# Performance work log

Hardware: AMD Instinct MI355X
Metric: run time of the kernel (lower is better)

Reference implementation:

```python
import jax, jax.numpy as jnp
import numpy as np

B, N, U = 8, 2048, 256
BN_EPS = 1e-3  # keras BatchNormalization default epsilon
ADJ_DENSITY = 0.008  # ~16 neighbors per node on average


def setup_inputs() -> dict:
    key = jax.random.key(0)
    ks = jax.random.split(key, 16)
    s = 0.05  # weight scale ('random_normal' init is small-stddev in keras)
    x = jax.random.normal(ks[0], (B, N, U), jnp.float32)
    # sparse binary adjacency stored dense (per-sample SpMM pattern)
    adj = (jax.random.uniform(ks[1], (B, N, N)) < ADJ_DENSITY).astype(jnp.float32)
    nodal_mask = jnp.ones((B, N), jnp.float32)
    return {
        'x': x, 'adj': adj, 'nodal_mask': nodal_mask,
        'W_lin': jax.random.normal(ks[2], (U, U)) * s, 'b_lin': jnp.zeros((U,)),
        'Wq_mp': jax.random.normal(ks[3], (3, U, U)) * s, 'bq_mp': jnp.zeros((3, U)),
        'Wk_mp': jax.random.normal(ks[4], (3, U, U)) * s, 'bk_mp': jnp.zeros((3, U)),
        'Wv_mp': jax.random.normal(ks[5], (3, U, U)) * s, 'bv_mp': jnp.zeros((3, U)),
        'Wk_att': jax.random.normal(ks[6], (U, U)) * s,
        'Wv_att': jax.random.normal(ks[7], (U, U)) * s,
        'Wq_att': jax.random.normal(ks[8], (U, U)) * s,
        'Wo_att': jax.random.normal(ks[9], (U, U)) * s,
        'bn_gamma': jnp.ones((U,)), 'bn_beta': jnp.zeros((U,)),
        'bn_mean': jnp.zeros((U,)), 'bn_var': jnp.ones((U,)),
        'W_proj': jax.random.normal(ks[10], (U, U)) * s, 'b_proj': jnp.zeros((U,)),
        'W_res': jax.random.normal(ks[11], (U, U)) * s, 'b_res': jnp.zeros((U,)),
    }


def _dympn(x, adj, Ws, bs, mask):
    # 3 message-passing layers, each applied K_l=2 times (inference value)
    for i in range(3):
        for _ in range(2):
            xn = jnp.einsum('bmn,bnd->bmd', adj, x)  # batched SpMM (graph_conv mode)
            x = jax.nn.silu(jnp.einsum('bmd,de->bme', xn, Ws[i]) + bs[i])
    return x * mask[:, :, None]


def reference(x, adj, nodal_mask, W_lin, b_lin, Wq_mp, bq_mp, Wk_mp, bk_mp,
              Wv_mp, bv_mp, Wk_att, Wv_att, Wq_att, Wo_att,
              bn_gamma, bn_beta, bn_mean, bn_var, W_proj, b_proj, W_res, b_res):
    initial_x = x
    adj = jax.lax.stop_gradient(adj)
    h = jnp.einsum('bnd,de->bne', x, W_lin) + b_lin
    q = _dympn(h, adj, Wq_mp, bq_mp, nodal_mask)
    k = _dympn(h, adj, Wk_mp, bk_mp, nodal_mask)
    v = _dympn(h, adj, Wv_mp, bv_mp, nodal_mask)
    # linear attention
    m = nodal_mask[:, :, None]
    pk = jax.nn.silu(jnp.einsum('bnd,de->bne', k, Wk_att) * m)
    pv = jnp.einsum('bnd,de->bne', v, Wv_att) * m
    pq = jnp.einsum('bnd,de->bne', q, Wq_att)
    kv = jnp.einsum('bnd,bne->bde', pk, pv)       # [B,U,U]
    attn = jnp.einsum('bnd,bde->bne', pq, kv)
    attn = jnp.einsum('bnd,de->bne', attn, Wo_att)
    # batch norm (inference: moving stats) over last axis
    y = attn + initial_x
    y = bn_gamma * (y - bn_mean) * jax.lax.rsqrt(bn_var + BN_EPS) + bn_beta
    out = jax.nn.silu(jnp.einsum('bnd,de->bne', y, W_proj) + b_proj)
    out = out + jnp.einsum('bnd,de->bne', initial_x, W_res) + b_res
    out = out * nodal_mask[:, :, None]
    return out
```

## Files before the change

kernel.cpp:

```cpp
#include <hip/hip_runtime.h>
#include <stdint.h>

#define NB 8
#define NN 2048
#define NU 256
#define CAP 64
#define BNEPS 0.001f
#define GSTR ((size_t)(NN * NU + 256))

typedef __attribute__((ext_vector_type(8))) short short8;
typedef __attribute__((ext_vector_type(4))) float floatx4;
typedef unsigned short u16;
typedef unsigned int u32;
typedef unsigned long long u64;

__device__ __forceinline__ float bf2f(u16 u) {
  union { u32 i; float f; } c; c.i = ((u32)u) << 16; return c.f;
}
__device__ __forceinline__ u16 f2bf(float f) {
  union { float f; u32 i; } c; c.f = f;
  return (u16)((c.i + 0x7fffu + ((c.i >> 16) & 1u)) >> 16);
}
__device__ __forceinline__ void splitbf(float a, u16& h, u16& l) {
  h = f2bf(a);
  l = f2bf(a - bf2f(h));
}

enum : unsigned {
  F_BIAS = 2u, F_SILU = 4u, F_MASKPRE = 8u, F_MASKPOST = 16u,
  F_ADDX = 32u, F_BN = 64u, F_ADDT = 128u, F_BPERMAT = 512u,
  F_TPLANES = 1024u, F_OUTHL = 2048u, F_NTOUT = 4096u, F_GSTRIDE = 8192u
};

#define TP_MAT 524288
#define TP_LO  4194304
#define MSZ ((size_t)NN * NU)

struct WPtrs { const float* p[16]; };

__global__ __launch_bounds__(256) void prologue_k(
    WPtrs wp, u16* __restrict__ wdst,
    const float* __restrict__ x, u16* __restrict__ xdst, size_t xLo,
    const float* __restrict__ adj, int* __restrict__ cnt, int* __restrict__ idx,
    float* __restrict__ ga, float* __restrict__ gb)
{
  int bid = blockIdx.x;
  int tid = threadIdx.x;
  __shared__ int c0;
  if (bid < 512) {
    int gid = bid * 256 + tid;
    int mat = gid >> 13;
    int rem = gid & 8191;
    int kb = rem >> 10;
    int n = (rem >> 2) & 255;
    int slot = rem & 3;
    int qv = (slot - (n >> 1)) & 3;
    int k0 = kb * 32 + qv * 8;
    const float* W = wp.p[mat];
    u32 oh[4], ol[4];
#pragma unroll
    for (int t2 = 0; t2 < 4; t2++) {
      float f0 = W[(size_t)(k0 + 2 * t2) * 256 + n];
      float f1 = W[(size_t)(k0 + 2 * t2 + 1) * 256 + n];
      u16 h0, l0, h1, l1;
      splitbf(f0, h0, l0);
      splitbf(f1, h1, l1);
      oh[t2] = (u32)h0 | ((u32)h1 << 16);
      ol[t2] = (u32)l0 | ((u32)l1 << 16);
    }
    uint4 qh; qh.x = oh[0]; qh.y = oh[1]; qh.z = oh[2]; qh.w = oh[3];
    uint4 ql; ql.x = ol[0]; ql.y = ol[1]; ql.z = ol[2]; ql.w = ol[3];
    *(uint4*)(wdst + (size_t)gid * 8) = qh;
    *(uint4*)(wdst + 1048576 + (size_t)gid * 8) = ql;
  } else if (bid < 4608) {
    size_t i = ((size_t)(bid - 512) * 256 + tid) * 4;
    float4 v = *(const float4*)(x + i);
    u16 h0, l0, h1, l1, h2, l2, h3, l3;
    splitbf(v.x, h0, l0); splitbf(v.y, h1, l1);
    splitbf(v.z, h2, l2); splitbf(v.w, h3, l3);
    uint2 H; H.x = (u32)h0 | ((u32)h1 << 16); H.y = (u32)h2 | ((u32)h3 << 16);
    uint2 L; L.x = (u32)l0 | ((u32)l1 << 16); L.y = (u32)l2 | ((u32)l3 << 16);
    *(uint2*)(xdst + i) = H;
    *(uint2*)(xdst + xLo + i) = L;
  } else if (bid < 20992) {
    int row = bid - 4608;
    const float* base = adj + (size_t)row * NN;
    if (tid == 0) c0 = 0;
    __syncthreads();
#pragma unroll
    for (int j = 0; j < 8; j++) {
      int n = j * 256 + tid;
      if (base[n] != 0.f) {
        int p = atomicAdd(&c0, 1);
        if (p < CAP) idx[(size_t)row * CAP + p] = n;
      }
    }
    __syncthreads();
    int cc = (c0 < CAP ? c0 : CAP);
    for (int p = cc + tid; p < CAP; p += 256) idx[(size_t)row * CAP + p] = -1;
    if (tid == 0) cnt[row] = cc;
  } else {
    int g = bid - 20992;
    float* base = (g < 24 ? ga : gb) + (size_t)(g % 24) * GSTR;
    base[tid] = 0.f;
  }
}

template <unsigned F>
__device__ __forceinline__ void gemm_epi(
    floatx4 (&acc)[2][2], int b, int bm, int w, int m16, int q,
    const float* __restrict__ bias, const float* __restrict__ mask,
    const float* __restrict__ xf32,
    const float* __restrict__ gma, const float* __restrict__ bta,
    const float* __restrict__ bmu, const float* __restrict__ bvr,
    const float* __restrict__ addt, void* __restrict__ outp, size_t oLo)
{
#pragma unroll
  for (int mt = 0; mt < 2; mt++) {
    if (F & F_TPLANES) {
      u16* oh = (u16*)outp + (size_t)b * TP_MAT;
      u16* ol = oh + TP_LO;
      int gr0 = bm + mt * 16 + q * 4;
#pragma unroll
      for (int nt = 0; nt < 2; nt++) {
        int col = w * 32 + nt * 16 + m16;
        u16 hh[4], ll[4];
#pragma unroll
        for (int r = 0; r < 4; r++) {
          float t2 = acc[mt][nt][r];
          float mv = mask[b * NN + gr0 + r];
          if (F & F_MASKPRE) t2 *= mv;
          if (F & F_SILU) t2 = t2 / (1.f + __expf(-t2));
          if (F & F_MASKPOST) t2 *= mv;
          splitbf(t2, hh[r], ll[r]);
        }
        uint2 H2, L2v;
        H2.x = (u32)hh[0] | ((u32)hh[1] << 16);
        H2.y = (u32)hh[2] | ((u32)hh[3] << 16);
        L2v.x = (u32)ll[0] | ((u32)ll[1] << 16);
        L2v.y = (u32)ll[2] | ((u32)ll[3] << 16);
        if (F & F_NTOUT) {
          __builtin_nontemporal_store(*(u64*)&H2, (u64*)(oh + (size_t)col * 2048 + gr0));
          __builtin_nontemporal_store(*(u64*)&L2v, (u64*)(ol + (size_t)col * 2048 + gr0));
        } else {
          *(uint2*)(oh + (size_t)col * 2048 + gr0) = H2;
          *(uint2*)(ol + (size_t)col * 2048 + gr0) = L2v;
        }
      }
    } else {
#pragma unroll
      for (int r = 0; r < 4; r++) {
        int gr = bm + mt * 16 + q * 4 + r;
        float mval = 1.f;
        if (F & (F_MASKPRE | F_MASKPOST)) mval = mask[b * NN + gr];
#pragma unroll
        for (int nt = 0; nt < 2; nt++) {
          int col = w * 32 + nt * 16 + m16;
          float t2 = acc[mt][nt][r];
          if (F & F_BIAS) t2 += bias[col];
          if (F & F_MASKPRE) t2 *= mval;
          if (F & F_SILU) t2 = t2 / (1.f + __expf(-t2));
          if (F & F_ADDX) t2 += xf32[((size_t)b * NN + gr) * NU + col];
          if (F & F_BN) t2 = gma[col] * (t2 - bmu[col]) * rsqrtf(bvr[col] + BNEPS) + bta[col];
          if (F & F_ADDT) t2 += addt[((size_t)b * NN + gr) * NU + col];
          if (F & F_MASKPOST) t2 *= mval;
          size_t o;
          if (F & F_GSTRIDE) o = (size_t)b * GSTR + (size_t)gr * NU + col;
          else o = ((size_t)b * NN + gr) * NU + col;
          if (F & F_OUTHL) {
            u16 h0, l0;
            splitbf(t2, h0, l0);
            if (F & F_NTOUT) {
              __builtin_nontemporal_store(h0, (u16*)outp + o);
              __builtin_nontemporal_store(l0, (u16*)outp + o + oLo);
            } else {
              ((u16*)outp)[o] = h0;
              ((u16*)outp)[o + oLo] = l0;
            }
          } else {
            if (F & F_NTOUT) __builtin_nontemporal_store(t2, (float*)outp + o);
            else ((float*)outp)[o] = t2;
          }
        }
      }
    }
  }
}

template <int NG, unsigned SF, unsigned F0, unsigned F1, unsigned F2, bool DK = false>
__global__ __launch_bounds__(512, 8) void gemm_k(
    const u16* __restrict__ A0, const u16* __restrict__ A1, const u16* __restrict__ A2,
    size_t aLo,
    const u16* __restrict__ W0, const u16* __restrict__ W1, const u16* __restrict__ W2,
    size_t wLo,
    const float* __restrict__ b0, const float* __restrict__ b1, const float* __restrict__ b2,
    const float* __restrict__ mask,
    const float* __restrict__ xf32,
    const float* __restrict__ gma, const float* __restrict__ bta,
    const float* __restrict__ bmu, const float* __restrict__ bvr,
    const float* __restrict__ addt,
    void* __restrict__ o0, void* __restrict__ o1, void* __restrict__ o2,
    size_t oLo,
    const float* __restrict__ gsrc,
    const float* __restrict__ sb0, const float* __restrict__ sb1, const float* __restrict__ sb2,
    const int* __restrict__ ncnt, const int* __restrict__ nidx)
{
  const int tid = threadIdx.x;
  const int id = blockIdx.x;
  const int xcd = id & 7;
  const int t = id >> 3;
  const int chain = (NG == 1) ? 0 : (t >> 6);
  const int xt = (NG == 1) ? t : (t & 63);
  const int b = xcd;
  const int bm = xt * 32;

  __shared__ alignas(16) u16 Ah[32 * 264];
  __shared__ alignas(16) u16 Al[32 * 264];

  const u16* Wsel = (chain == 0) ? W0 : (chain == 1 ? W1 : W2);
  if (F0 & F_BPERMAT) Wsel = W0 + (size_t)b * 65536;
  const u16* Whi = Wsel;
  const u16* Wlo = Whi + wLo;

  const int lane = tid & 63;
  const int w = tid >> 6;

  if constexpr (SF != 0u) {
    const float* __restrict__ gm = gsrc + (size_t)(chain * 8 + b) * GSTR + 256;
    const float* sb = (chain == 0) ? sb0 : (chain == 1 ? sb1 : sb2);
    const int c = lane * 4;
    float4 bb = *(const float4*)(sb + c);
    const int r0 = w * 4;
    const int* ips[4];
    float4 av[4];
    int rowids[4];
    int maxc = 0;
#pragma unroll
    for (int i = 0; i < 4; i++) {
      rowids[i] = b * NN + bm + r0 + i;
      int cn = ncnt[rowids[i]];
      maxc = cn > maxc ? cn : maxc;
      ips[i] = nidx + (size_t)rowids[i] * CAP;
      av[i].x = av[i].y = av[i].z = av[i].w = 0.f;
    }
    maxc = (maxc + 3) & ~3;
#pragma unroll 1
    for (int e = 0; e < maxc; e += 4) {
#pragma unroll
      for (int i = 0; i < 4; i++) {
        int4 i4 = *(const int4*)(ips[i] + e);
        float4 v0 = *(const float4*)(gm + (ptrdiff_t)i4.x * 256 + c);
        float4 v1 = *(const float4*)(gm + (ptrdiff_t)i4.y * 256 + c);
        float4 v2 = *(const float4*)(gm + (ptrdiff_t)i4.z * 256 + c);
        float4 v3 = *(const float4*)(gm + (ptrdiff_t)i4.w * 256 + c);
        av[i].x += v0.x + v1.x + v2.x + v3.x;
        av[i].y += v0.y + v1.y + v2.y + v3.y;
        av[i].z += v0.z + v1.z + v2.z + v3.z;
        av[i].w += v0.w + v1.w + v2.w + v3.w;
      }
    }
#pragma unroll
    for (int i = 0; i < 4; i++) {
      float ov[4] = {av[i].x + bb.x, av[i].y + bb.y, av[i].z + bb.z, av[i].w + bb.w};
      float mv = (SF & F_MASKPOST) ? mask[rowids[i]] : 1.f;
      u16 hh[4], ll[4];
#pragma unroll
      for (int j = 0; j < 4; j++) {
        float t2 = ov[j];
        if (SF & F_SILU) t2 = t2 / (1.f + __expf(-t2));
        if (SF & F_MASKPOST) t2 *= mv;
        splitbf(t2, hh[j], ll[j]);
      }
      uint2 H; H.x = (u32)hh[0] | ((u32)hh[1] << 16); H.y = (u32)hh[2] | ((u32)hh[3] << 16);
      uint2 L; L.x = (u32)ll[0] | ((u32)ll[1] << 16); L.y = (u32)ll[2] | ((u32)ll[3] << 16);
      *(uint2*)&Ah[(r0 + i) * 264 + c] = H;
      *(uint2*)&Al[(r0 + i) * 264 + c] = L;
    }
  } else {
    const u16* Abase = (chain == 0) ? A0 : (chain == 1 ? A1 : A2);
    const u16* Ahp = Abase + (size_t)b * MSZ;
    const u16* Alp = Ahp + aLo;
    {
      int s = tid;
      int r = s >> 4;
      int c = (s & 15) << 4;
      size_t ao = (size_t)(bm + r) * 256 + c;
      *(uint4*)&Ah[r * 264 + c] = *(const uint4*)(Ahp + ao);
      *(uint4*)&Ah[r * 264 + c + 8] = *(const uint4*)(Ahp + ao + 8);
      *(uint4*)&Al[r * 264 + c] = *(const uint4*)(Alp + ao);
      *(uint4*)&Al[r * 264 + c + 8] = *(const uint4*)(Alp + ao + 8);
    }
  }
  __syncthreads();

  const int m16 = lane & 15;
  const int q = lane >> 4;

  floatx4 acc[2][2];
#pragma unroll
  for (int i = 0; i < 2; i++)
#pragma unroll
    for (int j = 0; j < 2; j++) acc[i][j] = (floatx4){0.f, 0.f, 0.f, 0.f};

#pragma unroll
  for (int kk = 0; kk < 8; kk++) {
    short8 bh[2], bl2[2];
#pragma unroll
    for (int nt = 0; nt < 2; nt++) {
      int n = w * 32 + nt * 16 + m16;
      size_t off = (size_t)kk * 8192 + (size_t)n * 32 + (size_t)(((q + (n >> 1)) & 3) * 8);
      bh[nt] = *(const short8*)(Whi + off);
      bl2[nt] = *(const short8*)(Wlo + off);
    }
#pragma unroll
    for (int mt = 0; mt < 2; mt++) {
      int row = mt * 16 + m16;
      short8 ah = *(const short8*)&Ah[row * 264 + kk * 32 + q * 8];
      short8 al2 = *(const short8*)&Al[row * 264 + kk * 32 + q * 8];
#pragma unroll
      for (int nt = 0; nt < 2; nt++) {
        acc[mt][nt] = __builtin_amdgcn_mfma_f32_16x16x32_bf16(ah, bh[nt], acc[mt][nt], 0, 0, 0);
        acc[mt][nt] = __builtin_amdgcn_mfma_f32_16x16x32_bf16(al2, bh[nt], acc[mt][nt], 0, 0, 0);
        acc[mt][nt] = __builtin_amdgcn_mfma_f32_16x16x32_bf16(ah, bl2[nt], acc[mt][nt], 0, 0, 0);
      }
    }
  }

  if constexpr (DK) {
#pragma unroll
    for (int mt = 0; mt < 2; mt++)
#pragma unroll
      for (int nt = 0; nt < 2; nt++) {
        int col = w * 32 + nt * 16 + m16;
        float bp = b1[col];
#pragma unroll
        for (int r = 0; r < 4; r++) {
          float t2 = acc[mt][nt][r] + bp;
          acc[mt][nt][r] = t2 / (1.f + __expf(-t2));
        }
      }
    __syncthreads();
    {
      const u16* Ahp = A1 + (size_t)b * MSZ;
      const u16* Alp = Ahp + aLo;
      int s = tid;
      int r = s >> 4;
      int c = (s & 15) << 4;
      size_t ao = (size_t)(bm + r) * 256 + c;
      *(uint4*)&Ah[r * 264 + c] = *(const uint4*)(Ahp + ao);
      *(uint4*)&Ah[r * 264 + c + 8] = *(const uint4*)(Ahp + ao + 8);
      *(uint4*)&Al[r * 264 + c] = *(const uint4*)(Alp + ao);
      *(uint4*)&Al[r * 264 + c + 8] = *(const uint4*)(Alp + ao + 8);
    }
    __syncthreads();
    const u16* W1h = W1;
    const u16* W1l = W1 + wLo;
#pragma unroll
    for (int kk = 0; kk < 8; kk++) {
      short8 bh[2], bl2[2];
#pragma unroll
      for (int nt = 0; nt < 2; nt++) {
        int n = w * 32 + nt * 16 + m16;
        size_t off = (size_t)kk * 8192 + (size_t)n * 32 + (size_t)(((q + (n >> 1)) & 3) * 8);
        bh[nt] = *(const short8*)(W1h + off);
        bl2[nt] = *(const short8*)(W1l + off);
      }
#pragma unroll
      for (int mt = 0; mt < 2; mt++) {
        int row = mt * 16 + m16;
        short8 ah = *(const short8*)&Ah[row * 264 + kk * 32 + q * 8];
        short8 al2 = *(const short8*)&Al[row * 264 + kk * 32 + q * 8];
#pragma unroll
        for (int nt = 0; nt < 2; nt++) {
          acc[mt][nt] = __builtin_amdgcn_mfma_f32_16x16x32_bf16(ah, bh[nt], acc[mt][nt], 0, 0, 0);
          acc[mt][nt] = __builtin_amdgcn_mfma_f32_16x16x32_bf16(al2, bh[nt], acc[mt][nt], 0, 0, 0);
          acc[mt][nt] = __builtin_amdgcn_mfma_f32_16x16x32_bf16(ah, bl2[nt], acc[mt][nt], 0, 0, 0);
        }
      }
    }
  }

  if (NG == 1 || chain == 0)
    gemm_epi<F0>(acc, b, bm, w, m16, q, b0, mask, xf32, gma, bta, bmu, bvr, addt, o0, oLo);
  else if (chain == 1)
    gemm_epi<F1>(acc, b, bm, w, m16, q, b1, mask, xf32, gma, bta, bmu, bvr, addt, o1, oLo);
  else
    gemm_epi<F2>(acc, b, bm, w, m16, q, b2, mask, xf32, gma, bta, bmu, bvr, addt, o2, oLo);
}

__global__ __launch_bounds__(256, 2) void kv_k(
    const u16* __restrict__ pkT, const u16* __restrict__ pvT, float* __restrict__ part)
{
  int et = blockIdx.x * 128;
  int dt = blockIdx.y * 128;
  int z = blockIdx.z;
  int b = z & 7;
  int p = z >> 3;
  int tid = threadIdx.x;
  int lane = tid & 63, w = tid >> 6;
  int m16 = lane & 15, q = lane >> 4;

  const u16* pkh = pkT + (size_t)b * TP_MAT;
  const u16* pkl = pkh + TP_LO;
  const u16* pvh = pvT + (size_t)b * TP_MAT;
  const u16* pvl = pvh + TP_LO;

  int d_base = dt + (w >> 1) * 64 + m16;
  int e_base = et + (w & 1) * 64 + m16;

  floatx4 acc[4][4];
#pragma unroll
  for (int i = 0; i < 4; i++)
#pragma unroll
    for (int j = 0; j < 4; j++) acc[i][j] = (floatx4){0.f, 0.f, 0.f, 0.f};

#pragma unroll
  for (int kt = 0; kt < 8; kt++) {
    int kc = p * 256 + kt * 32 + q * 8;
    short8 ah[4], al[4], bh[4], bl[4];
#pragma unroll
    for (int mt = 0; mt < 4; mt++) {
      size_t o = (size_t)(d_base + mt * 16) * 2048 + kc;
      ah[mt] = *(const short8*)(pkh + o);
      al[mt] = *(const short8*)(pkl + o);
    }
#pragma unroll
    for (int nt = 0; nt < 4; nt++) {
      size_t o = (size_t)(e_base + nt * 16) * 2048 + kc;
      bh[nt] = *(const short8*)(pvh + o);
      bl[nt] = *(const short8*)(pvl + o);
    }
#pragma unroll
    for (int mt = 0; mt < 4; mt++)
#pragma unroll
      for (int nt = 0; nt < 4; nt++) {
        acc[mt][nt] = __builtin_amdgcn_mfma_f32_16x16x32_bf16(ah[mt], bh[nt], acc[mt][nt], 0, 0, 0);
        acc[mt][nt] = __builtin_amdgcn_mfma_f32_16x16x32_bf16(al[mt], bh[nt], acc[mt][nt], 0, 0, 0);
        acc[mt][nt] = __builtin_amdgcn_mfma_f32_16x16x32_bf16(ah[mt], bl[nt], acc[mt][nt], 0, 0, 0);
      }
  }

#pragma unroll
  for (int mt = 0; mt < 4; mt++)
#pragma unroll
    for (int r = 0; r < 4; r++) {
      int d = dt + (w >> 1) * 64 + mt * 16 + q * 4 + r;
#pragma unroll
      for (int nt = 0; nt < 4; nt++) {
        int e = et + (w & 1) * 64 + nt * 16 + m16;
        __builtin_nontemporal_store(acc[mt][nt][r],
                                    &part[(size_t)z * 65536 + (size_t)d * 256 + e]);
      }
    }
}

__global__ __launch_bounds__(256) void kv_conv_k(const float* __restrict__ part, u16* __restrict__ dst)
{
  int gid = blockIdx.x * 256 + threadIdx.x;
  int b = gid >> 13;
  int rem = gid & 8191;
  int kb = rem >> 10;
  int e = (rem >> 2) & 255;
  int slot = rem & 3;
  int qv = (slot - (e >> 1)) & 3;
  int d0 = kb * 32 + qv * 8;
  const float* src = part + (size_t)b * 65536 + (size_t)d0 * 256 + e;
  u32 oh[4], ol[4];
#pragma unroll
  for (int t2 = 0; t2 < 4; t2++) {
    float s0 = 0.f, s1 = 0.f;
#pragma unroll
    for (int pp = 0; pp < 8; pp++) {
      const float* sp = src + (size_t)pp * 524288 + t2 * 512;
      s0 += sp[0];
      s1 += sp[256];
    }
    u16 h0, l0, h1, l1;
    splitbf(s0, h0, l0);
    splitbf(s1, h1, l1);
    oh[t2] = (u32)h0 | ((u32)h1 << 16);
    ol[t2] = (u32)l0 | ((u32)l1 << 16);
  }
  uint4 qh; qh.x = oh[0]; qh.y = oh[1]; qh.z = oh[2]; qh.w = oh[3];
  uint4 ql; ql.x = ol[0]; ql.y = ol[1]; ql.z = ol[2]; ql.w = ol[3];
  *(uint4*)(dst + (size_t)gid * 8) = qh;
  *(uint4*)(dst + 524288 + (size_t)gid * 8) = ql;
}

extern "C" void kernel_launch(void* const* d_in, const int* in_sizes, int n_in,
                              void* d_out, int out_size, void* d_ws, size_t ws_size,
                              hipStream_t stream)
{
  const float* x = (const float*)d_in[0];
  const float* adj = (const float*)d_in[1];
  const float* mask = (const float*)d_in[2];
  const float* W_lin = (const float*)d_in[3];
  const float* b_lin = (const float*)d_in[4];
  const float* Wq_mp = (const float*)d_in[5];
  const float* bq_mp = (const float*)d_in[6];
  const float* Wk_mp = (const float*)d_in[7];
  const float* bk_mp = (const float*)d_in[8];
  const float* Wv_mp = (const float*)d_in[9];
  const float* bv_mp = (const float*)d_in[10];
  const float* Wk_att = (const float*)d_in[11];
  const float* Wv_att = (const float*)d_in[12];
  const float* Wq_att = (const float*)d_in[13];
  const float* Wo_att = (const float*)d_in[14];
  const float* bn_gamma = (const float*)d_in[15];
  const float* bn_beta = (const float*)d_in[16];
  const float* bn_mean = (const float*)d_in[17];
  const float* bn_var = (const float*)d_in[18];
  const float* W_proj = (const float*)d_in[19];
  const float* b_proj = (const float*)d_in[20];
  const float* W_res = (const float*)d_in[21];
  const float* b_res = (const float*)d_in[22];

  char* ws = (char*)d_ws;
  int* CNT    = (int*)(ws + 0);
  int* IDX    = (int*)(ws + (1ull << 20));
  u16* WSZ    = (u16*)(ws + (5ull << 20));
  u16* KVS    = (u16*)(ws + (9ull << 20));
  float* KVP  = (float*)(ws + (11ull << 20));
  u16* XHL    = (u16*)(ws + (27ull << 20));
  u16* HHL    = (u16*)(ws + (43ull << 20));
  float* GA   = (float*)(ws + (59ull << 20));
  float* GB   = (float*)(ws + (110ull << 20));
  u16* PKT    = (u16*)(ws + (161ull << 20));
  u16* PVT    = (u16*)(ws + (177ull << 20));
  u16* ATT    = (u16*)(ws + (193ull << 20));
  u16* YHL    = (u16*)(ws + (209ull << 20));

  const size_t WLO = 1048576;
  const size_t KLO = 524288;
  const size_t A8  = 8 * MSZ;
  const unsigned FG = F_NTOUT | F_GSTRIDE;

  u16* PQHL = HHL;

  WPtrs wp;
  wp.p[0] = W_lin;
  wp.p[1] = Wq_mp; wp.p[2] = Wq_mp + 65536; wp.p[3] = Wq_mp + 131072;
  wp.p[4] = Wk_mp; wp.p[5] = Wk_mp + 65536; wp.p[6] = Wk_mp + 131072;
  wp.p[7] = Wv_mp; wp.p[8] = Wv_mp + 65536; wp.p[9] = Wv_mp + 131072;
  wp.p[10] = Wk_att; wp.p[11] = Wv_att; wp.p[12] = Wq_att; wp.p[13] = Wo_att;
  wp.p[14] = W_proj; wp.p[15] = W_res;
  prologue_k<<<21040, 256, 0, stream>>>(wp, WSZ, x, XHL, A8, adj, CNT, IDX, GA, GB);

  gemm_k<1, 0u, F_BIAS | F_OUTHL, 0u, 0u><<<512, 512, 0, stream>>>(
      XHL, XHL, XHL, A8, WSZ, WSZ, WSZ, WLO,
      b_lin, nullptr, nullptr, mask, nullptr,
      bn_gamma, bn_beta, bn_mean, bn_var, nullptr,
      HHL, nullptr, nullptr, A8,
      nullptr, nullptr, nullptr, nullptr, CNT, IDX);

  gemm_k<3, 0u, FG, FG, FG><<<1536, 512, 0, stream>>>(
      HHL, HHL, HHL, A8,
      WSZ + (size_t)1 * 65536, WSZ + (size_t)4 * 65536, WSZ + (size_t)7 * 65536, WLO,
      nullptr, nullptr, nullptr, mask, nullptr,
      bn_gamma, bn_beta, bn_mean, bn_var, nullptr,
      GA + 256, GA + 8 * GSTR + 256, GA + 16 * GSTR + 256, 0,
      nullptr, nullptr, nullptr, nullptr, CNT, IDX);

  for (int s = 1; s < 6; s++) {
    int iw = s >> 1;
    int ib = (s - 1) >> 1;
    float* Gin = (s & 1) ? GA : GB;
    float* Gout = (s & 1) ? GB : GA;
    gemm_k<3, F_BIAS | F_SILU, FG, FG, FG><<<1536, 512, 0, stream>>>(
        nullptr, nullptr, nullptr, 0,
        WSZ + (size_t)(1 + iw) * 65536, WSZ + (size_t)(4 + iw) * 65536,
        WSZ + (size_t)(7 + iw) * 65536, WLO,
        nullptr, nullptr, nullptr, mask, nullptr,
        bn_gamma, bn_beta, bn_mean, bn_var, nullptr,
        Gout + 256, Gout + 8 * GSTR + 256, Gout + 16 * GSTR + 256, 0,
        Gin, bq_mp + ib * 256, bk_mp + ib * 256, bv_mp + ib * 256, CNT, IDX);
  }

  gemm_k<3, F_BIAS | F_SILU | F_MASKPOST,
         F_OUTHL | F_NTOUT, F_SILU | F_MASKPRE | F_TPLANES | F_NTOUT,
         F_MASKPOST | F_TPLANES | F_NTOUT>
      <<<1536, 512, 0, stream>>>(
      nullptr, nullptr, nullptr, 0,
      WSZ + (size_t)12 * 65536, WSZ + (size_t)10 * 65536, WSZ + (size_t)11 * 65536, WLO,
      nullptr, nullptr, nullptr, mask, nullptr,
      bn_gamma, bn_beta, bn_mean, bn_var, nullptr,
      PQHL, PKT, PVT, A8,
      GB, bq_mp + 512, bk_mp + 512, bv_mp + 512, CNT, IDX);

  kv_k<<<dim3(2, 2, 64), 256, 0, stream>>>(PKT, PVT, KVP);
  kv_conv_k<<<256, 256, 0, stream>>>(KVP, KVS);

  gemm_k<1, 0u, F_BPERMAT | F_OUTHL, 0u, 0u><<<512, 512, 0, stream>>>(
      PQHL, PQHL, PQHL, A8, KVS, KVS, KVS, KLO,
      nullptr, nullptr, nullptr, mask, nullptr,
      bn_gamma, bn_beta, bn_mean, bn_var, nullptr,
      ATT, nullptr, nullptr, A8,
      nullptr, nullptr, nullptr, nullptr, CNT, IDX);

  gemm_k<1, 0u, F_ADDX | F_BN | F_OUTHL, 0u, 0u><<<512, 512, 0, stream>>>(
      ATT, ATT, ATT, A8,
      WSZ + (size_t)13 * 65536, nullptr, nullptr, WLO,
      nullptr, nullptr, nullptr, mask, x,
      bn_gamma, bn_beta, bn_mean, bn_var, nullptr,
      YHL, nullptr, nullptr, A8,
      nullptr, nullptr, nullptr, nullptr, CNT, IDX);

  gemm_k<1, 0u, F_BIAS | F_MASKPOST, 0u, 0u, true><<<512, 512, 0, stream>>>(
      YHL, XHL, YHL, A8,
      WSZ + (size_t)14 * 65536, WSZ + (size_t)15 * 65536, nullptr, WLO,
      b_res, b_proj, nullptr, mask, nullptr,
      bn_gamma, bn_beta, bn_mean, bn_var, nullptr,
      d_out, nullptr, nullptr, 0,
      nullptr, nullptr, nullptr, nullptr, CNT, IDX);

  (void)in_sizes; (void)n_in; (void)out_size; (void)ws_size;
}
```

Baseline: 883.5 us.

## Double GEMM row tile to 64, drop nontemporal stores, refine SpMM gather

Doubles the rows each GEMM block handles from 32 to 64, so every loaded weight fragment feeds twice as many MFMA tiles, and halves the grid sizes to match. Launch bounds drop to 4 waves-per-EU occupancy and LDS use doubles. All nontemporal stores become ordinary stores so intermediate outputs can stay in cache for the next kernel. The gather step now handles 8 rows per wave with per-row count guards and a scalar tail, replacing padded -1 index loads, at the cost of more branching and fewer blocks to hide latency.

```diff
diff --git a/kernel.cpp b/kernel.cpp
--- a/kernel.cpp
+++ b/kernel.cpp
@@ -29,7 +29,7 @@
 enum : unsigned {
   F_BIAS = 2u, F_SILU = 4u, F_MASKPRE = 8u, F_MASKPOST = 16u,
   F_ADDX = 32u, F_BN = 64u, F_ADDT = 128u, F_BPERMAT = 512u,
-  F_TPLANES = 1024u, F_OUTHL = 2048u, F_NTOUT = 4096u, F_GSTRIDE = 8192u
+  F_TPLANES = 1024u, F_OUTHL = 2048u, F_GSTRIDE = 8192u
 };
 
 #define TP_MAT 524288
@@ -108,7 +108,7 @@
 
 template <unsigned F>
 __device__ __forceinline__ void gemm_epi(
-    floatx4 (&acc)[2][2], int b, int bm, int w, int m16, int q,
+    floatx4 (&acc)[4][2], int b, int bm, int w, int m16, int q,
     const float* __restrict__ bias, const float* __restrict__ mask,
     const float* __restrict__ xf32,
     const float* __restrict__ gma, const float* __restrict__ bta,
@@ -116,7 +116,7 @@
     const float* __restrict__ addt, void* __restrict__ outp, size_t oLo)
 {
 #pragma unroll
-  for (int mt = 0; mt < 2; mt++) {
+  for (int mt = 0; mt < 4; mt++) {
     if (F & F_TPLANES) {
       u16* oh = (u16*)outp + (size_t)b * TP_MAT;
       u16* ol = oh + TP_LO;
@@ -139,13 +139,8 @@
         H2.y = (u32)hh[2] | ((u32)hh[3] << 16);
         L2v.x = (u32)ll[0] | ((u32)ll[1] << 16);
         L2v.y = (u32)ll[2] | ((u32)ll[3] << 16);
-        if (F & F_NTOUT) {
-          __builtin_nontemporal_store(*(u64*)&H2, (u64*)(oh + (size_t)col * 2048 + gr0));
-          __builtin_nontemporal_store(*(u64*)&L2v, (u64*)(ol + (size_t)col * 2048 + gr0));
-        } else {
-          *(uint2*)(oh + (size_t)col * 2048 + gr0) = H2;
-          *(uint2*)(ol + (size_t)col * 2048 + gr0) = L2v;
-        }
+        *(uint2*)(oh + (size_t)col * 2048 + gr0) = H2;
+        *(uint2*)(ol + (size_t)col * 2048 + gr0) = L2v;
       }
     } else {
 #pragma unroll
@@ -170,16 +165,10 @@
           if (F & F_OUTHL) {
             u16 h0, l0;
             splitbf(t2, h0, l0);
-            if (F & F_NTOUT) {
-              __builtin_nontemporal_store(h0, (u16*)outp + o);
-              __builtin_nontemporal_store(l0, (u16*)outp + o + oLo);
-            } else {
-              ((u16*)outp)[o] = h0;
-              ((u16*)outp)[o + oLo] = l0;
-            }
+            ((u16*)outp)[o] = h0;
+            ((u16*)outp)[o + oLo] = l0;
           } else {
-            if (F & F_NTOUT) __builtin_nontemporal_store(t2, (float*)outp + o);
-            else ((float*)outp)[o] = t2;
+            ((float*)outp)[o] = t2;
           }
         }
       }
@@ -188,7 +177,7 @@
 }
 
 template <int NG, unsigned SF, unsigned F0, unsigned F1, unsigned F2, bool DK = false>
-__global__ __launch_bounds__(512, 8) void gemm_k(
+__global__ __launch_bounds__(512, 4) void gemm_k(
     const u16* __restrict__ A0, const u16* __restrict__ A1, const u16* __restrict__ A2,
     size_t aLo,
     const u16* __restrict__ W0, const u16* __restrict__ W1, const u16* __restrict__ W2,
@@ -209,13 +198,13 @@
   const int id = blockIdx.x;
   const int xcd = id & 7;
   const int t = id >> 3;
-  const int chain = (NG == 1) ? 0 : (t >> 6);
-  const int xt = (NG == 1) ? t : (t & 63);
+  const int chain = (NG == 1) ? 0 : (t >> 5);
+  const int xt = (NG == 1) ? t : (t & 31);
   const int b = xcd;
-  const int bm = xt * 32;
-
-  __shared__ alignas(16) u16 Ah[32 * 264];
-  __shared__ alignas(16) u16 Al[32 * 264];
+  const int bm = xt * 64;
+
+  __shared__ alignas(16) u16 Ah[64 * 264];
+  __shared__ alignas(16) u16 Al[64 * 264];
 
   const u16* Wsel = (chain == 0) ? W0 : (chain == 1 ? W1 : W2);
   if (F0 & F_BPERMAT) Wsel = W0 + (size_t)b * 65536;
@@ -230,39 +219,47 @@
     const float* sb = (chain == 0) ? sb0 : (chain == 1 ? sb1 : sb2);
     const int c = lane * 4;
     float4 bb = *(const float4*)(sb + c);
-    const int r0 = w * 4;
-    const int* ips[4];
-    float4 av[4];
-    int rowids[4];
+    const int r0 = w * 8;
+    const int* ips[8];
+    float4 av[8];
+    int cnts[8];
     int maxc = 0;
 #pragma unroll
-    for (int i = 0; i < 4; i++) {
-      rowids[i] = b * NN + bm + r0 + i;
-      int cn = ncnt[rowids[i]];
+    for (int i = 0; i < 8; i++) {
+      int rowid = b * NN + bm + r0 + i;
+      int cn = ncnt[rowid];
       maxc = cn > maxc ? cn : maxc;
-      ips[i] = nidx + (size_t)rowids[i] * CAP;
+      cnts[i] = cn;
+      ips[i] = nidx + (size_t)rowid * CAP;
       av[i].x = av[i].y = av[i].z = av[i].w = 0.f;
     }
-    maxc = (maxc + 3) & ~3;
-#pragma unroll 1
-    for (int e = 0; e < maxc; e += 4) {
-#pragma unroll
-      for (int i = 0; i < 4; i++) {
-        int4 i4 = *(const int4*)(ips[i] + e);
-        float4 v0 = *(const float4*)(gm + (ptrdiff_t)i4.x * 256 + c);
-        float4 v1 = *(const float4*)(gm + (ptrdiff_t)i4.y * 256 + c);
-        float4 v2 = *(const float4*)(gm + (ptrdiff_t)i4.z * 256 + c);
-        float4 v3 = *(const float4*)(gm + (ptrdiff_t)i4.w * 256 + c);
-        av[i].x += v0.x + v1.x + v2.x + v3.x;
-        av[i].y += v0.y + v1.y + v2.y + v3.y;
-        av[i].z += v0.z + v1.z + v2.z + v3.z;
-        av[i].w += v0.w + v1.w + v2.w + v3.w;
-      }
-    }
-#pragma unroll
-    for (int i = 0; i < 4; i++) {
+    for (int e = 0; e + 4 <= maxc; e += 4) {
+#pragma unroll
+      for (int i = 0; i < 8; i++) {
+        if (e + 4 <= cnts[i]) {
+          int4 i4 = *(const int4*)(ips[i] + e);
+          float4 v0 = *(const float4*)(gm + ((size_t)i4.x << 8) + c);
+          float4 v1 = *(const float4*)(gm + ((size_t)i4.y << 8) + c);
+          float4 v2 = *(const float4*)(gm + ((size_t)i4.z << 8) + c);
+          float4 v3 = *(const float4*)(gm + ((size_t)i4.w << 8) + c);
+          av[i].x += v0.x + v1.x + v2.x + v3.x;
+          av[i].y += v0.y + v1.y + v2.y + v3.y;
+          av[i].z += v0.z + v1.z + v2.z + v3.z;
+          av[i].w += v0.w + v1.w + v2.w + v3.w;
+        }
+      }
+    }
+#pragma unroll
+    for (int i = 0; i < 8; i++) {
+      for (int e = cnts[i] & ~3; e < cnts[i]; e++) {
+        float4 v = *(const float4*)(gm + ((size_t)ips[i][e] << 8) + c);
+        av[i].x += v.x; av[i].y += v.y; av[i].z += v.z; av[i].w += v.w;
+      }
+    }
+#pragma unroll
+    for (int i = 0; i < 8; i++) {
       float ov[4] = {av[i].x + bb.x, av[i].y + bb.y, av[i].z + bb.z, av[i].w + bb.w};
-      float mv = (SF & F_MASKPOST) ? mask[rowids[i]] : 1.f;
+      float mv = (SF & F_MASKPOST) ? mask[b * NN + bm + r0 + i] : 1.f;
       u16 hh[4], ll[4];
 #pragma unroll
       for (int j = 0; j < 4; j++) {
@@ -280,8 +277,8 @@
     const u16* Abase = (chain == 0) ? A0 : (chain == 1 ? A1 : A2);
     const u16* Ahp = Abase + (size_t)b * MSZ;
     const u16* Alp = Ahp + aLo;
-    {
-      int s = tid;
+#pragma unroll
+    for (int s = tid; s < 1024; s += 512) {
       int r = s >> 4;
       int c = (s & 15) << 4;
       size_t ao = (size_t)(bm + r) * 256 + c;
@@ -296,9 +293,9 @@
   const int m16 = lane & 15;
   const int q = lane >> 4;
 
-  floatx4 acc[2][2];
-#pragma unroll
-  for (int i = 0; i < 2; i++)
+  floatx4 acc[4][2];
+#pragma unroll
+  for (int i = 0; i < 4; i++)
 #pragma unroll
     for (int j = 0; j < 2; j++) acc[i][j] = (floatx4){0.f, 0.f, 0.f, 0.f};
 
@@ -313,7 +310,7 @@
       bl2[nt] = *(const short8*)(Wlo + off);
     }
 #pragma unroll
-    for (int mt = 0; mt < 2; mt++) {
+    for (int mt = 0; mt < 4; mt++) {
       int row = mt * 16 + m16;
       short8 ah = *(const short8*)&Ah[row * 264 + kk * 32 + q * 8];
       short8 al2 = *(const short8*)&Al[row * 264 + kk * 32 + q * 8];
@@ -328,7 +325,7 @@
 
   if constexpr (DK) {
 #pragma unroll
-    for (int mt = 0; mt < 2; mt++)
+    for (int mt = 0; mt < 4; mt++)
 #pragma unroll
       for (int nt = 0; nt < 2; nt++) {
         int col = w * 32 + nt * 16 + m16;
@@ -343,14 +340,16 @@
     {
       const u16* Ahp = A1 + (size_t)b * MSZ;
       const u16* Alp = Ahp + aLo;
-      int s = tid;
-      int r = s >> 4;
-      int c = (s & 15) << 4;
-      size_t ao = (size_t)(bm + r) * 256 + c;
-      *(uint4*)&Ah[r * 264 + c] = *(const uint4*)(Ahp + ao);
-      *(uint4*)&Ah[r * 264 + c + 8] = *(const uint4*)(Ahp + ao + 8);
-      *(uint4*)&Al[r * 264 + c] = *(const uint4*)(Alp + ao);
-      *(uint4*)&Al[r * 264 + c + 8] = *(const uint4*)(Alp + ao + 8);
+#pragma unroll
+      for (int s = tid; s < 1024; s += 512) {
+        int r = s >> 4;
+        int c = (s & 15) << 4;
+        size_t ao = (size_t)(bm + r) * 256 + c;
+        *(uint4*)&Ah[r * 264 + c] = *(const uint4*)(Ahp + ao);
+        *(uint4*)&Ah[r * 264 + c + 8] = *(const uint4*)(Ahp + ao + 8);
+        *(uint4*)&Al[r * 264 + c] = *(const uint4*)(Alp + ao);
+        *(uint4*)&Al[r * 264 + c + 8] = *(const uint4*)(Alp + ao + 8);
+      }
     }
     __syncthreads();
     const u16* W1h = W1;
@@ -366,7 +365,7 @@
         bl2[nt] = *(const short8*)(W1l + off);
       }
 #pragma unroll
-      for (int mt = 0; mt < 2; mt++) {
+      for (int mt = 0; mt < 4; mt++) {
         int row = mt * 16 + m16;
         short8 ah = *(const short8*)&Ah[row * 264 + kk * 32 + q * 8];
         short8 al2 = *(const short8*)&Al[row * 264 + kk * 32 + q * 8];
@@ -448,8 +447,7 @@
 #pragma unroll
       for (int nt = 0; nt < 4; nt++) {
         int e = et + (w & 1) * 64 + nt * 16 + m16;
-        __builtin_nontemporal_store(acc[mt][nt][r],
-                                    &part[(size_t)z * 65536 + (size_t)d * 256 + e]);
+        part[(size_t)z * 65536 + (size_t)d * 256 + e] = acc[mt][nt][r];
       }
     }
 }
@@ -533,7 +531,7 @@
   const size_t WLO = 1048576;
   const size_t KLO = 524288;
   const size_t A8  = 8 * MSZ;
-  const unsigned FG = F_NTOUT | F_GSTRIDE;
+  const unsigned FG = F_GSTRIDE;
 
   u16* PQHL = HHL;
 
@@ -546,14 +544,14 @@
   wp.p[14] = W_proj; wp.p[15] = W_res;
   prologue_k<<<21040, 256, 0, stream>>>(wp, WSZ, x, XHL, A8, adj, CNT, IDX, GA, GB);
 
-  gemm_k<1, 0u, F_BIAS | F_OUTHL, 0u, 0u><<<512, 512, 0, stream>>>(
+  gemm_k<1, 0u, F_BIAS | F_OUTHL, 0u, 0u><<<256, 512, 0, stream>>>(
       XHL, XHL, XHL, A8, WSZ, WSZ, WSZ, WLO,
       b_lin, nullptr, nullptr, mask, nullptr,
       bn_gamma, bn_beta, bn_mean, bn_var, nullptr,
       HHL, nullptr, nullptr, A8,
       nullptr, nullptr, nullptr, nullptr, CNT, IDX);
 
-  gemm_k<3, 0u, FG, FG, FG><<<1536, 512, 0, stream>>>(
+  gemm_k<3, 0u, FG, FG, FG><<<768, 512, 0, stream>>>(
       HHL, HHL, HHL, A8,
       WSZ + (size_t)1 * 65536, WSZ + (size_t)4 * 65536, WSZ + (size_t)7 * 65536, WLO,
       nullptr, nullptr, nullptr, mask, nullptr,
@@ -566,7 +564,7 @@
     int ib = (s - 1) >> 1;
     float* Gin = (s & 1) ? GA : GB;
     float* Gout = (s & 1) ? GB : GA;
-    gemm_k<3, F_BIAS | F_SILU, FG, FG, FG><<<1536, 512, 0, stream>>>(
+    gemm_k<3, F_BIAS | F_SILU, FG, FG, FG><<<768, 512, 0, stream>>>(
         nullptr, nullptr, nullptr, 0,
         WSZ + (size_t)(1 + iw) * 65536, WSZ + (size_t)(4 + iw) * 65536,
         WSZ + (size_t)(7 + iw) * 65536, WLO,
@@ -577,9 +575,8 @@
   }
 
   gemm_k<3, F_BIAS | F_SILU | F_MASKPOST,
-         F_OUTHL | F_NTOUT, F_SILU | F_MASKPRE | F_TPLANES | F_NTOUT,
-         F_MASKPOST | F_TPLANES | F_NTOUT>
-      <<<1536, 512, 0, stream>>>(
+         F_OUTHL, F_SILU | F_MASKPRE | F_TPLANES, F_MASKPOST | F_TPLANES>
+      <<<768, 512, 0, stream>>>(
       nullptr, nullptr, nullptr, 0,
       WSZ + (size_t)12 * 65536, WSZ + (size_t)10 * 65536, WSZ + (size_t)11 * 65536, WLO,
       nullptr, nullptr, nullptr, mask, nullptr,
@@ -590,14 +587,14 @@
   kv_k<<<dim3(2, 2, 64), 256, 0, stream>>>(PKT, PVT, KVP);
   kv_conv_k<<<256, 256, 0, stream>>>(KVP, KVS);
 
-  gemm_k<1, 0u, F_BPERMAT | F_OUTHL, 0u, 0u><<<512, 512, 0, stream>>>(
+  gemm_k<1, 0u, F_BPERMAT | F_OUTHL, 0u, 0u><<<256, 512, 0, stream>>>(
       PQHL, PQHL, PQHL, A8, KVS, KVS, KVS, KLO,
       nullptr, nullptr, nullptr, mask, nullptr,
       bn_gamma, bn_beta, bn_mean, bn_var, nullptr,
       ATT, nullptr, nullptr, A8,
       nullptr, nullptr, nullptr, nullptr, CNT, IDX);
 
-  gemm_k<1, 0u, F_ADDX | F_BN | F_OUTHL, 0u, 0u><<<512, 512, 0, stream>>>(
+  gemm_k<1, 0u, F_ADDX | F_BN | F_OUTHL, 0u, 0u><<<256, 512, 0, stream>>>(
       ATT, ATT, ATT, A8,
       WSZ + (size_t)13 * 65536, nullptr, nullptr, WLO,
       nullptr, nullptr, nullptr, mask, x,
@@ -605,7 +602,7 @@
       YHL, nullptr, nullptr, A8,
       nullptr, nullptr, nullptr, nullptr, CNT, IDX);
 
-  gemm_k<1, 0u, F_BIAS | F_MASKPOST, 0u, 0u, true><<<512, 512, 0, stream>>>(
+  gemm_k<1, 0u, F_BIAS | F_MASKPOST, 0u, 0u, true><<<256, 512, 0, stream>>>(
       YHL, XHL, YHL, A8,
       WSZ + (size_t)14 * 65536, WSZ + (size_t)15 * 65536, nullptr, WLO,
       b_res, b_proj, nullptr, mask, nullptr,
```

New measurement: 779.1 us. -11.8%, faster.
